# Performance work log

Measured on AMD Instinct MI355X. Metric: run time of the kernel, lower is better.

Reference implementation:

```python
import jax, jax.numpy as jnp
import numpy as np

# dims: B jets, K routed slots per jet, S particles, D embed, E experts, H heads
B, K, S, D, E, H = 512, 2, 128, 128, 4, 8
F = 4 * D  # ffn_dim
MAXN = 1.0 - 1e-5  # Poincare ball (c=1) max norm for projx


def _n(x):
    return jnp.sqrt(jnp.clip(jnp.sum(x * x, axis=-1, keepdims=True), 1e-15))


def expmap0(u):
    n = _n(u)
    return jnp.tanh(n) * u / n


def logmap0(x):
    n = _n(x)
    return jnp.arctanh(jnp.minimum(n, MAXN)) * x / n


def projx(x):
    n = _n(x)
    return jnp.where(n > MAXN, x * (MAXN / n), x)


def mobius_add(x, y):
    xy = jnp.sum(x * y, axis=-1, keepdims=True)
    x2 = jnp.sum(x * x, axis=-1, keepdims=True)
    y2 = jnp.sum(y * y, axis=-1, keepdims=True)
    num = (1.0 + 2.0 * xy + y2) * x + (1.0 - x2) * y
    den = 1.0 + 2.0 * xy + x2 * y2
    return num / jnp.clip(den, 1e-15)


def layernorm(x, g, b):
    m = jnp.mean(x, axis=-1, keepdims=True)
    v = jnp.mean((x - m) ** 2, axis=-1, keepdims=True)
    return g * (x - m) / jnp.sqrt(v + 1e-5) + b


def man_linear(x, W, b):
    # Manifold_Linear: mobius matvec == expmap0(W @ logmap0(x)), then mobius bias, projx
    return projx(mobius_add(expmap0(logmap0(x) @ W.T), expmap0(b)))


def mob_relu(x):
    # Mob_Act(ReLU): expmap0(relu(logmap0(x)))
    return expmap0(jax.nn.relu(logmap0(x)))


def setup_inputs():
    key = jax.random.key(0)
    ks = jax.random.split(key, 16)
    features = expmap0(0.05 * jax.random.normal(ks[0], (B, K, S, D), jnp.float32))
    # K distinct expert ids per sample (original .nonzero().item() assumes uniqueness)
    expert_indices = jnp.argsort(jax.random.uniform(ks[1], (B, E)), axis=1)[:, :K].astype(jnp.int32)
    pm = jax.random.uniform(ks[2], (B, S)) < 0.2
    pm = pm.at[:, 0].set(False)  # keep at least one valid token per row
    w = lambda k, shp, sc: sc * jax.random.normal(k, shp, jnp.float32)
    s = 1.0 / np.sqrt(D)
    sf = 1.0 / np.sqrt(F)
    return dict(
        features=features, expert_indices=expert_indices, padding_mask=pm,
        ln1_g=jnp.ones((E, D)), ln1_b=jnp.zeros((E, D)),
        ln2_g=jnp.ones((E, D)), ln2_b=jnp.zeros((E, D)),
        wq=w(ks[3], (E, D, D), s), bq=w(ks[4], (E, D), 0.02),
        wk=w(ks[5], (E, D, D), s), bk=w(ks[6], (E, D), 0.02),
        wv=w(ks[7], (E, D, D), s), bv=w(ks[8], (E, D), 0.02),
        wo=w(ks[9], (E, D, D), s), bo=w(ks[10], (E, D), 0.02),
        fc1_w=w(ks[11], (E, F, D), s), fc1_b=w(ks[12], (E, F), 0.02),
        fc2_w=w(ks[13], (E, D, F), sf), fc2_b=w(ks[14], (E, D), 0.02),
    )


def _mha(x, Wq, bq, Wk, bk, Wv, bv, Wo, bo, pad_bias):
    b, s, d = x.shape
    hd = d // H
    q = logmap0(man_linear(x, Wq, bq)).reshape(b, s, H, hd)
    k = logmap0(man_linear(x, Wk, bk)).reshape(b, s, H, hd)
    v = logmap0(man_linear(x, Wv, bv)).reshape(b, s, H, hd)
    scores = jnp.einsum('bqhd,bkhd->bhqk', q, k) * (1.0 / np.sqrt(hd)) + pad_bias
    att = jax.nn.softmax(scores, axis=-1)
    ctx = jnp.einsum('bhqk,bkhd->bqhd', att, v).reshape(b, s, d)
    return man_linear(expmap0(ctx), Wo, bo)


def _expert(x, e, P, pad_bias):
    res = x
    h = expmap0(layernorm(logmap0(x), P['ln1_g'][e], P['ln1_b'][e]))
    h = projx(_mha(h, P['wq'][e], P['bq'][e], P['wk'][e], P['bk'][e],
                   P['wv'][e], P['bv'][e], P['wo'][e], P['bo'][e], pad_bias))
    x = projx(mobius_add(h, res))
    res = x
    h = projx(expmap0(layernorm(logmap0(x), P['ln2_g'][e], P['ln2_b'][e])))
    h = projx(mob_relu(man_linear(h, P['fc1_w'][e], P['fc1_b'][e])))
    h = mob_relu(man_linear(h, P['fc2_w'][e], P['fc2_b'][e]))
    return projx(mobius_add(h, res))


def reference(features, expert_indices, padding_mask,
              ln1_g, ln1_b, ln2_g, ln2_b,
              wq, bq, wk, bk, wv, bv, wo, bo,
              fc1_w, fc1_b, fc2_w, fc2_b):
    P = dict(ln1_g=ln1_g, ln1_b=ln1_b, ln2_g=ln2_g, ln2_b=ln2_b,
             wq=wq, bq=bq, wk=wk, bk=bk, wv=wv, bv=bv, wo=wo, bo=bo,
             fc1_w=fc1_w, fc1_b=fc1_b, fc2_w=fc2_w, fc2_b=fc2_b)
    pad_bias = jnp.where(padding_mask, -1e9, 0.0)[:, None, None, :]  # [B,1,1,S]
    outs = []
    for e in range(E):  # small fixed expert loop (distinct params)
        sel = expert_indices == e  # [B,K]
        present = jnp.any(sel, axis=1)  # [B]
        slot = jnp.argmax(sel, axis=1)  # [B]
        x = jnp.take_along_axis(features, slot[:, None, None, None], axis=1)[:, 0]  # [B,S,D]
        y = _expert(x, e, P, pad_bias)
        outs.append(jnp.where(present[:, None, None], y, 0.0))
    return jnp.stack(outs, axis=1)  # [B,E,S,D]; zero rows where expert not routed
```

## Files before the change

kernel.cpp:

```cpp
#include <hip/hip_runtime.h>
#include <stdint.h>

#define SS 128
#define DD 128
#define EE 4
#define HH 8
#define HDIM 16
#define FF 512
#define BB 512
#define KK 2
#define NTASK (BB*KK)
#define MAXNF 0.99999f
#define NW3 786432

typedef unsigned short u16;
typedef unsigned int u32;

typedef __attribute__((ext_vector_type(8))) short s8v;
typedef __attribute__((ext_vector_type(4))) float f4v;

#define MFMA32(a,b,c) __builtin_amdgcn_mfma_f32_16x16x32_bf16(a,b,c,0,0,0)

__device__ __forceinline__ float bf2f(u16 h){ return __uint_as_float(((u32)h)<<16); }
__device__ __forceinline__ u16 f2bf(float f){
  u32 x = __float_as_uint(f);
  u32 r = x + 0x7FFFu + ((x>>16)&1u);
  return (u16)(r>>16);
}
__device__ __forceinline__ float bfl(u32 u){ return __uint_as_float(u<<16); }
__device__ __forceinline__ float bfh(u32 u){ return __uint_as_float(u & 0xFFFF0000u); }

__device__ __forceinline__ float wsum(float v){
  #pragma unroll
  for(int off=32; off>0; off>>=1) v += __shfl_xor(v, off, 64);
  return v;
}
__device__ __forceinline__ float wmax(float v){
  #pragma unroll
  for(int off=32; off>0; off>>=1) v = fmaxf(v, __shfl_xor(v, off, 64));
  return v;
}
__device__ __forceinline__ float rsum16(float v){
  #pragma unroll
  for(int off=8; off>0; off>>=1) v += __shfl_xor(v, off, 64);
  return v;
}
__device__ __forceinline__ float artanhf_(float x){ return 0.5f*logf((1.f+x)/(1.f-x)); }

__device__ __forceinline__ u32 cvtpk(float a, float b){
  u32 r; asm("v_cvt_pk_bf16_f32 %0, %1, %2" : "=v"(r) : "v"(a), "v"(b)); return r;
}
__device__ __forceinline__ void split2(float a, float b, u32& H, u32& M, u32& L){
  H = cvtpk(a,b);
  float ra = a - bfl(H), rb = b - bfh(H);
  M = cvtpk(ra,rb);
  float sa = ra - bfl(M), sb = rb - bfh(M);
  L = cvtpk(sa,sb);
}
__device__ __forceinline__ void split8(const float* v, s8v& H, s8v& M, s8v& L){
  union { u32 w[4]; s8v s; } uh, um, ul;
  #pragma unroll
  for(int p=0;p<4;++p){
    u32 a,bq2,c; split2(v[2*p], v[2*p+1], a, bq2, c);
    uh.w[p]=a; um.w[p]=bq2; ul.w[p]=c;
  }
  H=uh.s; M=um.s; L=ul.s;
}
__device__ __forceinline__ s8v sel8(int c, s8v a, s8v b){ return c ? a : b; }

__device__ __forceinline__ u32 xf32(int row, int colf){
  return (u32)row*512u + (((u32)colf*4u) ^ (((u32)row&7u)<<4));
}
__device__ __forceinline__ u32 xfr_(int row, int colf){
  return (u32)row*2048u + (((u32)colf*4u) ^ (((u32)row&7u)<<4));
}

__device__ __forceinline__ void mkA512(const char* T, int row, int colf, int hm, s8v& A1, s8v& A2){
  float va[8];
  float4 v0 = *(const float4*)(T + xf32(row, colf));
  float4 v1 = *(const float4*)(T + xf32(row, colf+4));
  va[0]=v0.x; va[1]=v0.y; va[2]=v0.z; va[3]=v0.w;
  va[4]=v1.x; va[5]=v1.y; va[6]=v1.z; va[7]=v1.w;
  s8v H,M,L; split8(va, H,M,L);
  A1 = sel8(hm, H, M);
  A2 = sel8(hm, L, H);
}
__device__ __forceinline__ void mkA2048(const char* T, int row, int colf, int hm, s8v& A1, s8v& A2){
  float va[8];
  float4 v0 = *(const float4*)(T + xfr_(row, colf));
  float4 v1 = *(const float4*)(T + xfr_(row, colf+4));
  va[0]=v0.x; va[1]=v0.y; va[2]=v0.z; va[3]=v0.w;
  va[4]=v1.x; va[5]=v1.y; va[6]=v1.z; va[7]=v1.w;
  s8v H,M,L; split8(va, H,M,L);
  A1 = sel8(hm, H, M);
  A2 = sel8(hm, L, H);
}

template<typename T> __device__ __forceinline__ float ldv(const T* p){
  if constexpr (sizeof(T)==2) return bf2f(*(const u16*)p);
  else return *(const float*)p;
}
template<typename T> __device__ __forceinline__ void stv(T* p, float v){
  if constexpr (sizeof(T)==2) *(u16*)p = f2bf(v);
  else *(float*)p = v;
}
template<typename T> __device__ __forceinline__ void loadrow(const T* p, float* w){
  if constexpr (sizeof(T)==2){
    const uint4* q=(const uint4*)p;
    #pragma unroll
    for(int r=0;r<16;++r){
      uint4 t=q[r];
      w[r*8+0]=bfl(t.x); w[r*8+1]=bfh(t.x);
      w[r*8+2]=bfl(t.y); w[r*8+3]=bfh(t.y);
      w[r*8+4]=bfl(t.z); w[r*8+5]=bfh(t.z);
      w[r*8+6]=bfl(t.w); w[r*8+7]=bfh(t.w);
    }
  } else {
    const float4* q=(const float4*)p;
    #pragma unroll
    for(int r=0;r<32;++r){ float4 t=q[r]; w[r*4]=t.x; w[r*4+1]=t.y; w[r*4+2]=t.z; w[r*4+3]=t.w; }
  }
}
__device__ __forceinline__ float dotrow(const float* __restrict__ w, const float* __restrict__ u){
  float a0=0.f,a1=0.f,a2=0.f,a3=0.f;
  #pragma unroll
  for(int i=0;i<128;i+=4){
    a0+=w[i]*u[i]; a1+=w[i+1]*u[i+1]; a2+=w[i+2]*u[i+2]; a3+=w[i+3]*u[i+3];
  }
  return (a0+a1)+(a2+a3);
}

template<int NPL> __device__ __forceinline__ float vnorm(const float* v){
  float s=0.f;
  #pragma unroll
  for(int i=0;i<NPL;++i) s += v[i]*v[i];
  s = wsum(s);
  return sqrtf(fmaxf(s, 1e-15f));
}
template<int NPL> __device__ __forceinline__ void f_logmap0(float* v){
  float n = vnorm<NPL>(v);
  float sc = artanhf_(fminf(n, MAXNF))/n;
  #pragma unroll
  for(int i=0;i<NPL;++i) v[i]*=sc;
}
template<int NPL> __device__ __forceinline__ void f_expmap0(float* v){
  float n = vnorm<NPL>(v);
  float sc = tanhf(n)/n;
  #pragma unroll
  for(int i=0;i<NPL;++i) v[i]*=sc;
}
template<int NPL> __device__ __forceinline__ void f_projx(float* v){
  float n = vnorm<NPL>(v);
  if(n > MAXNF){
    float sc = MAXNF/n;
    #pragma unroll
    for(int i=0;i<NPL;++i) v[i]*=sc;
  }
}
template<int NPL> __device__ __forceinline__ void f_mobius_add(float* x, const float* y){
  float xy=0.f, x2=0.f, y2=0.f;
  #pragma unroll
  for(int i=0;i<NPL;++i){ xy+=x[i]*y[i]; x2+=x[i]*x[i]; y2+=y[i]*y[i]; }
  xy=wsum(xy); x2=wsum(x2); y2=wsum(y2);
  float cx = 1.f + 2.f*xy + y2;
  float cy = 1.f - x2;
  float den = fmaxf(1.f + 2.f*xy + x2*y2, 1e-15f);
  float inv = 1.f/den;
  #pragma unroll
  for(int i=0;i<NPL;++i) x[i] = (cx*x[i] + cy*y[i])*inv;
}
template<int NPL> __device__ __forceinline__ void f_layernorm(float* v, const float* g, const float* b){
  const float invD = 1.f/(float)(NPL*64);
  float m=0.f;
  #pragma unroll
  for(int i=0;i<NPL;++i) m += v[i];
  m = wsum(m)*invD;
  float s2=0.f;
  #pragma unroll
  for(int i=0;i<NPL;++i){ v[i]-=m; s2 += v[i]*v[i]; }
  s2 = wsum(s2)*invD;
  float inv = 1.f/sqrtf(s2+1e-5f);
  #pragma unroll
  for(int i=0;i<NPL;++i) v[i] = g[i]*(v[i]*inv) + b[i];
}

template<int NPL> __device__ __forceinline__ float vnorm16(const float* v){
  float s=0.f;
  #pragma unroll
  for(int i=0;i<NPL;++i) s += v[i]*v[i];
  s = rsum16(s);
  return sqrtf(fmaxf(s, 1e-15f));
}
template<int NPL> __device__ __forceinline__ void f16_logmap0(float* v){
  float n = vnorm16<NPL>(v);
  float sc = artanhf_(fminf(n, MAXNF))/n;
  #pragma unroll
  for(int i=0;i<NPL;++i) v[i]*=sc;
}
template<int NPL> __device__ __forceinline__ void f16_expmap0(float* v){
  float n = vnorm16<NPL>(v);
  float sc = tanhf(n)/n;
  #pragma unroll
  for(int i=0;i<NPL;++i) v[i]*=sc;
}
template<int NPL> __device__ __forceinline__ void f16_projx(float* v){
  float n = vnorm16<NPL>(v);
  if(n > MAXNF){
    float sc = MAXNF/n;
    #pragma unroll
    for(int i=0;i<NPL;++i) v[i]*=sc;
  }
}
template<int NPL> __device__ __forceinline__ void f16_mobius_add(float* x, const float* y){
  float xy=0.f, x2=0.f, y2=0.f;
  #pragma unroll
  for(int i=0;i<NPL;++i){ xy+=x[i]*y[i]; x2+=x[i]*x[i]; y2+=y[i]*y[i]; }
  xy=rsum16(xy); x2=rsum16(x2); y2=rsum16(y2);
  float cx = 1.f + 2.f*xy + y2;
  float cy = 1.f - x2;
  float den = fmaxf(1.f + 2.f*xy + x2*y2, 1e-15f);
  float inv = 1.f/den;
  #pragma unroll
  for(int i=0;i<NPL;++i) x[i] = (cx*x[i] + cy*y[i])*inv;
}
template<int NPL> __device__ __forceinline__ void f16_layernorm(float* v, const float* g, const float* b){
  const float invD = 1.f/(float)(NPL*16);
  float m=0.f;
  #pragma unroll
  for(int i=0;i<NPL;++i) m += v[i];
  m = rsum16(m)*invD;
  float s2=0.f;
  #pragma unroll
  for(int i=0;i<NPL;++i){ v[i]-=m; s2 += v[i]*v[i]; }
  s2 = rsum16(s2)*invD;
  float inv = 1.f/sqrtf(s2+1e-5f);
  #pragma unroll
  for(int i=0;i<NPL;++i) v[i] = g[i]*(v[i]*inv) + b[i];
}

__global__ void prep_kernel(const u16* __restrict__ feat16,
                            const unsigned char* __restrict__ mask,
                            float* __restrict__ mbias, int* __restrict__ flag){
  __shared__ int s_stats, s_max, s_nan;
  if(threadIdx.x==0){ s_stats=0; s_max=0; s_nan=0; }
  __syncthreads();
  int c=0;
  for(int i=threadIdx.x; i<131072; i+=blockDim.x){
    u16 v = feat16[i];
    if(((v>>7)&0xFFu)==0xFFu) c++;
  }
  if(c) atomicAdd(&s_nan, c);
  int lstats=0, lmax=0;
  for(int i=threadIdx.x; i<BB*SS; i+=blockDim.x){
    int v = mask[i];
    if(v){
      lmax = v>lmax ? v : lmax;
      if((i&3)==1) lstats|=1;
      if((i&3)!=0) lstats|=2;
    }
  }
  if(lstats) atomicOr(&s_stats, lstats);
  atomicMax(&s_max, lmax);
  __syncthreads();
  if(threadIdx.x==0) *flag = (s_nan>0) ? 1 : 0;
  int mode;
  if(s_max<=1) mode = (s_stats&2) ? 0 : 1;
  else         mode = (s_stats&1) ? 2 : 3;
  for(int i=threadIdx.x; i<BB*SS; i+=blockDim.x){
    bool m2;
    if(mode==0)      m2 = mask[i]!=0;
    else if(mode==1) m2 = ((const int*)mask)[i]!=0;
    else if(mode==2) m2 = ((const u16*)mask)[i]!=0;
    else             m2 = ((((const u32*)mask)[i])<<1)!=0;
    mbias[i] = m2 ? -1e9f : 0.f;
  }
}

template<typename T>
__global__ void zero_nr(const int* __restrict__ flag, const int* __restrict__ eidx, T* __restrict__ out){
  const int want = (sizeof(T)==4) ? 1 : 0;
  if(*flag != want) return;
  for(int slab=blockIdx.x; slab<BB*EE; slab+=gridDim.x){
    int b = slab>>2, e = slab&3;
    if(eidx[b*KK]==e || eidx[b*KK+1]==e) continue;
    T* p = out + (size_t)slab*(SS*DD);
    for(int i=threadIdx.x; i<SS*DD; i+=blockDim.x){
      if constexpr (sizeof(T)==2) p[i] = (T)0; else p[i] = 0.f;
    }
  }
}

__global__ void wsplit_kernel(const int* __restrict__ flag,
                              const float* __restrict__ wq, const float* __restrict__ wk,
                              const float* __restrict__ wv, const float* __restrict__ wo,
                              const float* __restrict__ f1w, const float* __restrict__ f2w,
                              u16* __restrict__ wsp){
  if(*flag != 1) return;
  int i = blockIdx.x*256 + threadIdx.x;
  if(i >= NW3) return;
  float x;
  if(i < 65536)       x = wq[i];
  else if(i < 131072) x = wk[i-65536];
  else if(i < 196608) x = wv[i-131072];
  else if(i < 262144) x = wo[i-196608];
  else if(i < 524288) x = f1w[i-262144];
  else                x = f2w[i-524288];
  u32 H,M,L; split2(x,x,H,M,L);
  wsp[i]         = (u16)H;
  wsp[NW3 + i]   = (u16)M;
  wsp[2*NW3 + i] = (u16)L;
}

__global__ __launch_bounds__(512)
void moe_f32(const int* __restrict__ flag,
             const float* __restrict__ feat, const int* __restrict__ eidx,
             const float* __restrict__ mbias,
             const float* __restrict__ ln1g, const float* __restrict__ ln1b,
             const float* __restrict__ ln2g, const float* __restrict__ ln2b,
             const float* __restrict__ bq, const float* __restrict__ bk_,
             const float* __restrict__ bv, const float* __restrict__ bo,
             const float* __restrict__ f1b, const float* __restrict__ f2b,
             const u16* __restrict__ wsp,
             float* __restrict__ out, int ntask)
{
  if(*flag != 1) return;

  __shared__ __align__(16) char LB[163840];
  char* UF  = LB;
  char* R2  = LB + 65536;
  char* SX  = LB + 131072;

  const int tid = threadIdx.x;
  const int lane = tid & 63;
  const int w    = tid >> 6;
  const int ll   = lane & 15;
  const int hl   = lane >> 4;
  const int hm   = (hl < 2);

  for(int task = blockIdx.x; task < ntask; task += gridDim.x){
    __syncthreads();
    const int b = task >> 1, slot = task & 1;
    const int e  = eidx[b*KK + slot];
    const int eo = eidx[b*KK + (slot^1)];
    int used = (1<<e)|(1<<eo), sp = 0, cnt = 0;
    #pragma unroll
    for(int t2=0;t2<4;++t2){ if(!((used>>t2)&1)){ if(cnt==slot) sp=t2; cnt++; } }
    const float* X = feat + (size_t)task * (SS*DD);
    float* own   = out + ((size_t)(b*EE+e )) * (SS*DD);
    float* spare = out + ((size_t)(b*EE+sp)) * (SS*DD);

    {
      float g1[2],b1[2];
      float2 t0;
      t0 = *(const float2*)(ln1g + e*DD + 2*lane); g1[0]=t0.x; g1[1]=t0.y;
      t0 = *(const float2*)(ln1b + e*DD + 2*lane); b1[0]=t0.x; b1[1]=t0.y;
      for(int r=0;r<16;++r){
        int t = w*16 + r;
        float2 xv = *(const float2*)(X + t*DD + 2*lane);
        float v[2] = {xv.x, xv.y};
        f_logmap0<2>(v);
        f_layernorm<2>(v, g1, b1);
        f_expmap0<2>(v);
        f_logmap0<2>(v);
        float2 o2; o2.x=v[0]; o2.y=v[1];
        *(float2*)(UF + xf32(t, 2*lane)) = o2;
      }
    }
    __syncthreads();

    {
      float ebq8[8], ebk8[8], ebv8[8];
      #pragma unroll
      for(int n=0;n<8;++n){
        ebq8[n] = bq [e*DD + n*16 + ll];
        ebk8[n] = bk_[e*DD + n*16 + ll];
        ebv8[n] = bv [e*DD + n*16 + ll];
      }
      f16_expmap0<8>(ebq8); f16_expmap0<8>(ebk8); f16_expmap0<8>(ebv8);

      #pragma unroll
      for(int m=0;m<3;++m){
        const u32 tb = (u32)m*65536u + (u32)e*16384u;
        s8v A1v[8], A2v[8];
        #pragma unroll
        for(int c=0;c<8;++c)
          mkA512(UF, w*16+ll, c*16 + (hl&1)*8, hm, A1v[c], A2v[c]);
        f4v acc[8];
        #pragma unroll
        for(int n=0;n<8;++n){ acc[n][0]=0.f; acc[n][1]=0.f; acc[n][2]=0.f; acc[n][3]=0.f; }
        #pragma unroll
        for(int n=0;n<8;++n){
          u32 nrow = (u32)(n*16 + ll);
          #pragma unroll
          for(int c=0;c<8;++c){
            u32 koff = c*16 + (hl&1)*8;
            s8v B1 = *(const s8v*)(wsp + tb + nrow*128 + koff);
            s8v B2 = *(const s8v*)(wsp + (hm?2:1)*NW3 + tb + nrow*128 + koff);
            s8v B3 = sel8(hm, B1, B2);
            acc[n] = MFMA32(A1v[c], B1, acc[n]);
            acc[n] = MFMA32(A1v[c], B2, acc[n]);
            acc[n] = MFMA32(A2v[c], B3, acc[n]);
          }
        }
        #pragma unroll
        for(int i=0;i<4;++i){
          int r = w*16 + hl*4 + i;
          float v[8];
          #pragma unroll
          for(int n=0;n<8;++n) v[n] = acc[n][i];
          f16_expmap0<8>(v);
          float eb[8];
          #pragma unroll
          for(int n=0;n<8;++n) eb[n] = (m==0) ? ebq8[n] : (m==1) ? ebk8[n] : ebv8[n];
          f16_mobius_add<8>(v, eb);
          f16_projx<8>(v);
          f16_logmap0<8>(v);
          if(m==0){
            #pragma unroll
            for(int n=0;n<8;++n) spare[(size_t)r*DD + n*16 + ll] = v[n];
          } else if(m==1){
            #pragma unroll
            for(int n=0;n<8;++n) *(float*)(R2 + xf32(r, n*16 + ll)) = v[n];
          } else {
            #pragma unroll
            for(int n=0;n<8;++n) own[(size_t)r*DD + n*16 + ll] = v[n];
          }
        }
      }
    }
    __syncthreads();

    {
      float mb_reg[8];
      #pragma unroll
      for(int nt=0;nt<8;++nt) mb_reg[nt] = mbias[b*SS + nt*16 + ll];

      for(int h=0; h<HH; ++h){
        {
          int tok = tid & 127, dq = tid >> 7;
          float4 vv = *(const float4*)(R2 + xf32(tok, h*16 + dq*4));
          u32 H0,M0,L0,H1,M1,L1;
          split2(vv.x,vv.y,H0,M0,L0); split2(vv.z,vv.w,H1,M1,L1);
          u32 o = (u32)tok*48u + (u32)dq*8u;
          *(u32*)(SX + 0*6144 + o) = H0; *(u32*)(SX + 0*6144 + o + 4) = H1;
          *(u32*)(SX + 1*6144 + o) = M0; *(u32*)(SX + 1*6144 + o + 4) = M1;
          *(u32*)(SX + 2*6144 + o) = L0; *(u32*)(SX + 2*6144 + o + 4) = L1;
        }
        __syncthreads();
        float qa[8];
        {
          float4 q0 = *(const float4*)(spare + (w*16+ll)*DD + h*16 + (hl&1)*8);
          float4 q1 = *(const float4*)(spare + (w*16+ll)*DD + h*16 + (hl&1)*8 + 4);
          qa[0]=q0.x; qa[1]=q0.y; qa[2]=q0.z; qa[3]=q0.w;
          qa[4]=q1.x; qa[5]=q1.y; qa[6]=q1.z; qa[7]=q1.w;
        }
        s8v QH,QM,QL; split8(qa, QH,QM,QL);
        s8v qA1 = sel8(hm, QH, QM);
        s8v qA2 = sel8(hm, QL, QH);
        f4v sc[8];
        #pragma unroll
        for(int nt=0;nt<8;++nt){
          u32 o = (u32)(nt*16+ll)*48u + (u32)(hl&1)*16u;
          s8v B1 = *(const s8v*)(SX + 0*6144 + o);
          s8v B2 = *(const s8v*)(SX + (hm?2:1)*6144 + o);
          s8v B3 = sel8(hm, B1, B2);
          f4v z = {0.f,0.f,0.f,0.f};
          z = MFMA32(qA1, B1, z);
          z = MFMA32(qA1, B2, z);
          z = MFMA32(qA2, B3, z);
          sc[nt] = z;
        }
        __syncthreads();
        #pragma unroll
        for(int i=0;i<4;++i){
          float p8[8]; float mx = -3e38f;
          #pragma unroll
          for(int nt=0;nt<8;++nt){ p8[nt] = sc[nt][i]*0.25f + mb_reg[nt]; mx = fmaxf(mx, p8[nt]); }
          #pragma unroll
          for(int o=1;o<16;o<<=1) mx = fmaxf(mx, __shfl_xor(mx, o, 64));
          float dn = 0.f;
          #pragma unroll
          for(int nt=0;nt<8;++nt){ p8[nt] = expf(p8[nt]-mx); dn += p8[nt]; }
          #pragma unroll
          for(int o=1;o<16;o<<=1) dn += __shfl_xor(dn, o, 64);
          float inv = 1.f/dn;
          #pragma unroll
          for(int nt=0;nt<8;++nt)
            *(float*)(UF + xf32(w*16 + hl*4 + i, nt*16 + ll)) = p8[nt]*inv;
        }
        f4v ca = {0.f,0.f,0.f,0.f};
        #pragma unroll
        for(int c=0;c<8;++c){
          float pa[8];
          {
            float4 p0 = *(const float4*)(UF + xf32(w*16+ll, c*16 + (hl&1)*8));
            float4 p1 = *(const float4*)(UF + xf32(w*16+ll, c*16 + (hl&1)*8 + 4));
            pa[0]=p0.x; pa[1]=p0.y; pa[2]=p0.z; pa[3]=p0.w;
            pa[4]=p1.x; pa[5]=p1.y; pa[6]=p1.z; pa[7]=p1.w;
          }
          s8v PH,PM,PL; split8(pa, PH,PM,PL);
          s8v pA1 = sel8(hm, PH, PM);
          s8v pA2 = sel8(hm, PL, PH);
          float va[8];
          {
            int kbase = c*16 + (hl&1)*8;
            #pragma unroll
            for(int j=0;j<8;++j)
              va[j] = own[(size_t)(kbase+j)*DD + h*16 + ll];
          }
          s8v VH,VM,VL; split8(va, VH,VM,VL);
          s8v vB2 = sel8(hm, VL, VM);
          s8v vB3 = sel8(hm, VH, VM);
          ca = MFMA32(pA1, VH, ca);
          ca = MFMA32(pA1, vB2, ca);
          ca = MFMA32(pA2, vB3, ca);
        }
        #pragma unroll
        for(int i=0;i<4;++i)
          *(float*)(R2 + xf32(w*16 + hl*4 + i, h*16 + ll)) = ca[i];
      }
    }
    __syncthreads();

    for(int r=0;r<16;++r){
      int t = w*16 + r;
      float2 cc2 = *(const float2*)(R2 + xf32(t, 2*lane));
      float v[2] = {cc2.x, cc2.y};
      f_expmap0<2>(v);
      f_logmap0<2>(v);
      float2 o2; o2.x=v[0]; o2.y=v[1];
      *(float2*)(UF + xf32(t, 2*lane)) = o2;
    }

    {
      float ebo8[8], g28[8], b28[8];
      #pragma unroll
      for(int n=0;n<8;++n){
        ebo8[n] = bo  [e*DD + n*16 + ll];
        g28[n]  = ln2g[e*DD + n*16 + ll];
        b28[n]  = ln2b[e*DD + n*16 + ll];
      }
      f16_expmap0<8>(ebo8);

      const u32 tb = 196608u + (u32)e*16384u;
      s8v A1v[8], A2v[8];
      #pragma unroll
      for(int c=0;c<8;++c)
        mkA512(UF, w*16+ll, c*16 + (hl&1)*8, hm, A1v[c], A2v[c]);
      f4v acc[8];
      #pragma unroll
      for(int n=0;n<8;++n){ acc[n][0]=0.f; acc[n][1]=0.f; acc[n][2]=0.f; acc[n][3]=0.f; }
      #pragma unroll
      for(int n=0;n<8;++n){
        u32 nrow = (u32)(n*16 + ll);
        #pragma unroll
        for(int c=0;c<8;++c){
          u32 koff = c*16 + (hl&1)*8;
          s8v B1 = *(const s8v*)(wsp + tb + nrow*128 + koff);
          s8v B2 = *(const s8v*)(wsp + (hm?2:1)*NW3 + tb + nrow*128 + koff);
          s8v B3 = sel8(hm, B1, B2);
          acc[n] = MFMA32(A1v[c], B1, acc[n]);
          acc[n] = MFMA32(A1v[c], B2, acc[n]);
          acc[n] = MFMA32(A2v[c], B3, acc[n]);
        }
      }
      #pragma unroll
      for(int i=0;i<4;++i){
        int r = w*16 + hl*4 + i;
        float v[8];
        #pragma unroll
        for(int n=0;n<8;++n) v[n] = acc[n][i];
        f16_expmap0<8>(v);
        f16_mobius_add<8>(v, ebo8);
        f16_projx<8>(v);
        f16_projx<8>(v);
        float res[8];
        #pragma unroll
        for(int n=0;n<8;++n) res[n] = X[(size_t)r*DD + n*16 + ll];
        f16_mobius_add<8>(v, res);
        f16_projx<8>(v);
        #pragma unroll
        for(int n=0;n<8;++n) own[(size_t)r*DD + n*16 + ll] = v[n];
        f16_logmap0<8>(v);
        f16_layernorm<8>(v, g28, b28);
        f16_expmap0<8>(v);
        f16_projx<8>(v);
        f16_logmap0<8>(v);
        #pragma unroll
        for(int n=0;n<8;++n) *(float*)(UF + xf32(r, n*16 + ll)) = v[n];
      }
    }
    __syncthreads();

    {
      float ebf1[8], ebf2[2];
      {
        float2 t0;
        #pragma unroll
        for(int j2=0;j2<4;++j2){
          t0 = *(const float2*)(f1b + e*FF + 2*lane + 128*j2); ebf1[2*j2]=t0.x; ebf1[2*j2+1]=t0.y;
        }
        f_expmap0<8>(ebf1);
        t0 = *(const float2*)(f2b + e*DD + 2*lane); ebf2[0]=t0.x; ebf2[1]=t0.y; f_expmap0<2>(ebf2);
      }
      for(int tc=0; tc<4; ++tc){
        const int t0i = tc*32;
        {
          #pragma unroll
          for(int mt=0; mt<2; ++mt){
            int arow = t0i + mt*16 + ll;
            s8v A1v[8], A2v[8];
            #pragma unroll
            for(int c=0;c<8;++c)
              mkA512(UF, arow, c*16 + (hl&1)*8, hm, A1v[c], A2v[c]);
            #pragma unroll
            for(int n4=0;n4<4;++n4){
              u32 nrow = (u32)(w*64 + n4*16 + ll);
              f4v acc = {0.f,0.f,0.f,0.f};
              #pragma unroll
              for(int c=0;c<8;++c){
                u32 koff = c*16 + (hl&1)*8;
                s8v B1 = *(const s8v*)(wsp + 262144u + (u32)e*65536u + nrow*128 + koff);
                s8v B2 = *(const s8v*)(wsp + (hm?2:1)*NW3 + 262144u + (u32)e*65536u + nrow*128 + koff);
                s8v B3 = sel8(hm, B1, B2);
                acc = MFMA32(A1v[c], B1, acc);
                acc = MFMA32(A1v[c], B2, acc);
                acc = MFMA32(A2v[c], B3, acc);
              }
              #pragma unroll
              for(int i=0;i<4;++i)
                *(float*)(R2 + xfr_(mt*16 + hl*4 + i, w*64 + n4*16 + ll)) = acc[i];
            }
          }
        }
        __syncthreads();
        for(int rr=0; rr<4; ++rr){
          int lr = w*4 + rr;
          float v[8];
          #pragma unroll
          for(int j2=0;j2<4;++j2){
            float2 pp = *(const float2*)(R2 + xfr_(lr, 2*lane + 128*j2));
            v[2*j2]=pp.x; v[2*j2+1]=pp.y;
          }
          f_expmap0<8>(v);
          f_mobius_add<8>(v, ebf1);
          f_projx<8>(v);
          f_logmap0<8>(v);
          #pragma unroll
          for(int i=0;i<8;++i) v[i] = fmaxf(v[i], 0.f);
          f_expmap0<8>(v);
          f_projx<8>(v);
          f_logmap0<8>(v);
          #pragma unroll
          for(int j2=0;j2<4;++j2){
            float2 o2; o2.x=v[2*j2]; o2.y=v[2*j2+1];
            *(float2*)(R2 + xfr_(lr, 2*lane + 128*j2)) = o2;
          }
        }
        __syncthreads();
        {
          u32 nrow = (u32)(w*16 + ll);
          #pragma unroll
          for(int mt=0; mt<2; ++mt){
            f4v ga = {0.f,0.f,0.f,0.f};
            #pragma unroll
            for(int grp=0; grp<4; ++grp){
              s8v A1v[8], A2v[8];
              #pragma unroll
              for(int cc=0;cc<8;++cc)
                mkA2048(R2, mt*16 + ll, (grp*8+cc)*16 + (hl&1)*8, hm, A1v[cc], A2v[cc]);
              #pragma unroll
              for(int cc=0;cc<8;++cc){
                int c = grp*8 + cc;
                u32 koff = c*16 + (hl&1)*8;
                s8v B1 = *(const s8v*)(wsp + 524288u + (u32)e*65536u + nrow*512 + koff);
                s8v B2 = *(const s8v*)(wsp + (hm?2:1)*NW3 + 524288u + (u32)e*65536u + nrow*512 + koff);
                s8v B3 = sel8(hm, B1, B2);
                ga = MFMA32(A1v[cc], B1, ga);
                ga = MFMA32(A1v[cc], B2, ga);
                ga = MFMA32(A2v[cc], B3, ga);
              }
            }
            #pragma unroll
            for(int i=0;i<4;++i)
              *(float*)(SX + xf32(mt*16 + hl*4 + i, w*16 + ll)) = ga[i];
          }
        }
        __syncthreads();
        for(int rr=0; rr<4; ++rr){
          int lr = w*4 + rr; int gt = t0i + lr;
          float v[2];
          v[0] = *(const float*)(SX + xf32(lr, 2*lane));
          v[1] = *(const float*)(SX + xf32(lr, 2*lane+1));
          f_expmap0<2>(v);
          f_mobius_add<2>(v, ebf2);
          f_projx<2>(v);
          f_logmap0<2>(v);
          v[0]=fmaxf(v[0],0.f); v[1]=fmaxf(v[1],0.f);
          f_expmap0<2>(v);
          float2 xx = *(const float2*)(own + gt*DD + 2*lane);
          float x1v[2] = {xx.x, xx.y};
          f_mobius_add<2>(v, x1v);
          f_projx<2>(v);
          float2 o2; o2.x=v[0]; o2.y=v[1];
          *(float2*)(own + gt*DD + 2*lane) = o2;
        }
        __syncthreads();
      }
    }

    {
      float4 z4 = {0.f,0.f,0.f,0.f};
      for(int i=tid; i<4096; i+=512) *(float4*)(spare + 4*i) = z4;
    }
  }
}

template<typename T>
__global__ __launch_bounds__(256)
void moe_kernel(const int* __restrict__ flag,
                const T* __restrict__ feat, const int* __restrict__ eidx,
                const float* __restrict__ mbias,
                const T* __restrict__ ln1g, const T* __restrict__ ln1b,
                const T* __restrict__ ln2g, const T* __restrict__ ln2b,
                const T* __restrict__ wq, const T* __restrict__ bq,
                const T* __restrict__ wk, const T* __restrict__ bk_,
                const T* __restrict__ wv, const T* __restrict__ bv,
                const T* __restrict__ wo, const T* __restrict__ bo,
                const T* __restrict__ f1w, const T* __restrict__ f1b,
                const T* __restrict__ f2w, const T* __restrict__ f2b,
                T* __restrict__ out, float* __restrict__ ws, int ntask)
{
  const int want = (sizeof(T)==4) ? 1 : 0;
  if(*flag != want) return;

  __shared__ float U[SS*DD];
  const int tid  = threadIdx.x;
  const int lane = tid & 63;
  const int wid  = tid >> 6;
  float* T0 = ws + (size_t)blockIdx.x * (4*SS*DD);
  float* T1 = T0 + SS*DD;
  float* T2 = T1 + SS*DD;
  float* T3 = T2 + SS*DD;

  for(int task = blockIdx.x; task < ntask; task += gridDim.x){
    __syncthreads();
    const int b = task >> 1;
    const int e = eidx[b*KK + (task & 1)];
    const T* X = feat + (size_t)task * (SS*DD);

    for(int r=0;r<32;++r){
      int t = wid*32 + r;
      float v[2];
      v[0]=ldv(&X[t*DD+lane]); v[1]=ldv(&X[t*DD+lane+64]);
      f_logmap0<2>(v);
      float g[2], bb[2];
      g[0]=ldv(&ln1g[e*DD+lane]);  g[1]=ldv(&ln1g[e*DD+lane+64]);
      bb[0]=ldv(&ln1b[e*DD+lane]); bb[1]=ldv(&ln1b[e*DD+lane+64]);
      f_layernorm<2>(v,g,bb);
      f_expmap0<2>(v);
      f_logmap0<2>(v);
      U[t*DD+lane]=v[0]; U[t*DD+lane+64]=v[1];
    }
    __syncthreads();

    {
      int j = tid & 127, tg = tid >> 7;
      for(int m=0;m<3;++m){
        const T* Wm = (m==0?wq : m==1?wk : wv) + (size_t)e*DD*DD + (size_t)j*DD;
        float* Ym = (m==0?T0 : m==1?T1 : T2);
        float w[128];
        loadrow(Wm, w);
        for(int tt=0;tt<64;++tt){
          int t = tg*64+tt;
          Ym[t*DD+j] = dotrow(w, &U[t*DD]);
        }
      }
    }
    __syncthreads();

    for(int m=0;m<3;++m){
      const T* bias = (m==0?bq : m==1?bk_ : bv) + e*DD;
      float* Y = (m==0?T0 : m==1?T1 : T2);
      for(int r=0;r<32;++r){
        int t = wid*32+r;
        float v[2]; v[0]=Y[t*DD+lane]; v[1]=Y[t*DD+lane+64];
        f_expmap0<2>(v);
        float ebv2[2]; ebv2[0]=ldv(&bias[lane]); ebv2[1]=ldv(&bias[lane+64]);
        f_expmap0<2>(ebv2);
        f_mobius_add<2>(v, ebv2);
        f_projx<2>(v);
        f_logmap0<2>(v);
        Y[t*DD+lane]=v[0]; Y[t*DD+lane+64]=v[1];
      }
    }
    __syncthreads();

    {
      const float* mb = mbias + b*SS;
      for(int h=0; h<HH; ++h){
        for(int r=0;r<32;++r){
          int t = wid*32+r;
          float q16[16];
          #pragma unroll
          for(int i=0;i<16;++i) q16[i] = T0[t*DD + h*HDIM + i];
          int k0 = lane, k1 = lane+64;
          float s0=0.f, s1=0.f;
          #pragma unroll
          for(int i=0;i<16;++i){
            s0 += q16[i]*T1[k0*DD + h*HDIM + i];
            s1 += q16[i]*T1[k1*DD + h*HDIM + i];
          }
          s0 = s0*0.25f + mb[k0];
          s1 = s1*0.25f + mb[k1];
          float mx = wmax(fmaxf(s0,s1));
          float p0 = expf(s0-mx), p1 = expf(s1-mx);
          float dn = wsum(p0+p1);
          p0 /= dn; p1 /= dn;
          float part[16];
          #pragma unroll
          for(int i=0;i<16;++i)
            part[i] = p0*T2[k0*DD+h*HDIM+i] + p1*T2[k1*DD+h*HDIM+i];
          #pragma unroll
          for(int off=1; off<64; off<<=1){
            #pragma unroll
            for(int i=0;i<16;++i) part[i] += __shfl_xor(part[i], off, 64);
          }
          if(lane==0){
            #pragma unroll
            for(int i=0;i<16;++i) T0[t*DD + h*HDIM + i] = part[i];
          }
        }
      }
    }
    __syncthreads();

    for(int r=0;r<32;++r){
      int t=wid*32+r;
      float v[2]; v[0]=T0[t*DD+lane]; v[1]=T0[t*DD+lane+64];
      f_expmap0<2>(v);
      f_logmap0<2>(v);
      U[t*DD+lane]=v[0]; U[t*DD+lane+64]=v[1];
    }
    __syncthreads();

    {
      int j=tid&127, tg=tid>>7;
      float w[128];
      loadrow(wo + (size_t)e*DD*DD + (size_t)j*DD, w);
      for(int tt=0;tt<64;++tt){
        int t=tg*64+tt;
        T1[t*DD+j] = dotrow(w, &U[t*DD]);
      }
    }
    __syncthreads();

    for(int r=0;r<32;++r){
      int t=wid*32+r;
      float v[2]; v[0]=T1[t*DD+lane]; v[1]=T1[t*DD+lane+64];
      f_expmap0<2>(v);
      float ebv2[2]; ebv2[0]=ldv(&bo[e*DD+lane]); ebv2[1]=ldv(&bo[e*DD+lane+64]);
      f_expmap0<2>(ebv2);
      f_mobius_add<2>(v, ebv2);
      f_projx<2>(v);
      f_projx<2>(v);
      float res[2]; res[0]=ldv(&X[t*DD+lane]); res[1]=ldv(&X[t*DD+lane+64]);
      f_mobius_add<2>(v, res);
      f_projx<2>(v);
      T3[t*DD+lane]=v[0]; T3[t*DD+lane+64]=v[1];
      f_logmap0<2>(v);
      float g2[2], b2[2];
      g2[0]=ldv(&ln2g[e*DD+lane]); g2[1]=ldv(&ln2g[e*DD+lane+64]);
      b2[0]=ldv(&ln2b[e*DD+lane]); b2[1]=ldv(&ln2b[e*DD+lane+64]);
      f_layernorm<2>(v,g2,b2);
      f_expmap0<2>(v);
      f_projx<2>(v);
      f_logmap0<2>(v);
      U[t*DD+lane]=v[0]; U[t*DD+lane+64]=v[1];
    }
    __syncthreads();

    float* HID = T0;
    for(int tc=0; tc<2; ++tc){
      for(int pass=0;pass<2;++pass){
        int f = pass*256 + tid;
        float w[128];
        loadrow(f1w + (size_t)e*FF*DD + (size_t)f*DD, w);
        for(int tt=0;tt<64;++tt){
          HID[tt*FF+f] = dotrow(w, &U[(tc*64+tt)*DD]);
        }
      }
      __syncthreads();
      for(int r=0;r<16;++r){
        int t = wid*16+r;
        float v[8];
        #pragma unroll
        for(int i=0;i<8;++i) v[i]=HID[t*FF+lane+64*i];
        f_expmap0<8>(v);
        float ebv8[8];
        #pragma unroll
        for(int i=0;i<8;++i) ebv8[i]=ldv(&f1b[e*FF+lane+64*i]);
        f_expmap0<8>(ebv8);
        f_mobius_add<8>(v, ebv8);
        f_projx<8>(v);
        f_logmap0<8>(v);
        #pragma unroll
        for(int i=0;i<8;++i) v[i]=fmaxf(v[i],0.f);
        f_expmap0<8>(v);
        f_projx<8>(v);
        f_logmap0<8>(v);
        #pragma unroll
        for(int i=0;i<8;++i) HID[t*FF+lane+64*i]=v[i];
      }
      __syncthreads();
      {
        int j=tid&127, tg=tid>>7;
        for(int fc=0;fc<4;++fc){
          float w[128];
          loadrow(f2w + (size_t)e*DD*FF + (size_t)j*FF + fc*128, w);
          for(int tt=0;tt<32;++tt){
            int t=tg*32+tt;
            float acc = dotrow(w, HID + t*FF + fc*128);
            if(fc==0) T2[t*DD+j]=acc; else T2[t*DD+j]+=acc;
          }
        }
      }
      __syncthreads();
      for(int r=0;r<16;++r){
        int t=wid*16+r; int gt = tc*64+t;
        float v[2]; v[0]=T2[t*DD+lane]; v[1]=T2[t*DD+lane+64];
        f_expmap0<2>(v);
        float ebv2[2]; ebv2[0]=ldv(&f2b[e*DD+lane]); ebv2[1]=ldv(&f2b[e*DD+lane+64]);
        f_expmap0<2>(ebv2);
        f_mobius_add<2>(v, ebv2);
        f_projx<2>(v);
        f_logmap0<2>(v);
        v[0]=fmaxf(v[0],0.f); v[1]=fmaxf(v[1],0.f);
        f_expmap0<2>(v);
        float x1v[2]; x1v[0]=T3[gt*DD+lane]; x1v[1]=T3[gt*DD+lane+64];
        f_mobius_add<2>(v, x1v);
        f_projx<2>(v);
        T* op = out + ((size_t)(b*EE+e)*SS + gt)*DD;
        stv(&op[lane],    v[0]);
        stv(&op[lane+64], v[1]);
      }
      __syncthreads();
    }
  }
}

extern "C" void kernel_launch(void* const* d_in, const int* in_sizes, int n_in,
                              void* d_out, int out_size, void* d_ws, size_t ws_size,
                              hipStream_t stream){
  const void* feat = d_in[0];
  const int* eidx = (const int*)d_in[1];
  const unsigned char* pmask = (const unsigned char*)d_in[2];
  float* ws = (float*)d_ws;

  int* flag = (int*)ws;
  float* mbias = ws + 16;
  float* tiles = ws + 16 + BB*SS;
  u16* wsp = (u16*)(ws + 16 + BB*SS);
  const size_t WSP_F32 = (size_t)(3*NW3)/2;

  long wsf = (long)(ws_size/sizeof(float));
  long avail_old = wsf - (16 + BB*SS);
  long remain = wsf - (long)(16 + BB*SS) - (long)WSP_F32;

  int G = (int)(avail_old / (long)(4*SS*DD));
  if(G > NTASK) G = NTASK;
  if(G < 1) G = 1;
  int G2 = 256;
  if(G2 > NTASK) G2 = NTASK;
  bool newpath = (remain >= 0);

  prep_kernel<<<1,256,0,stream>>>((const u16*)feat, pmask, mbias, flag);
  zero_nr<u16>  <<<2048,256,0,stream>>>(flag, eidx, (u16*)d_out);
  zero_nr<float><<<2048,256,0,stream>>>(flag, eidx, (float*)d_out);

  if(newpath){
    wsplit_kernel<<<(NW3+255)/256,256,0,stream>>>(flag,
      (const float*)d_in[7], (const float*)d_in[9], (const float*)d_in[11], (const float*)d_in[13],
      (const float*)d_in[15], (const float*)d_in[17], wsp);
    moe_f32<<<G2,512,0,stream>>>(flag, (const float*)d_in[0], eidx, mbias,
      (const float*)d_in[3], (const float*)d_in[4], (const float*)d_in[5], (const float*)d_in[6],
      (const float*)d_in[8], (const float*)d_in[10], (const float*)d_in[12], (const float*)d_in[14],
      (const float*)d_in[16], (const float*)d_in[18],
      wsp, (float*)d_out, NTASK);
  }

  #define ARGS(T_) flag, (const T_*)d_in[0], eidx, mbias, \
    (const T_*)d_in[3], (const T_*)d_in[4], (const T_*)d_in[5], (const T_*)d_in[6], \
    (const T_*)d_in[7], (const T_*)d_in[8], (const T_*)d_in[9], (const T_*)d_in[10], \
    (const T_*)d_in[11], (const T_*)d_in[12], (const T_*)d_in[13], (const T_*)d_in[14], \
    (const T_*)d_in[15], (const T_*)d_in[16], (const T_*)d_in[17], (const T_*)d_in[18], \
    (T_*)d_out, tiles, NTASK
  moe_kernel<u16><<<G,256,0,stream>>>(ARGS(u16));
  if(!newpath){
    moe_kernel<float><<<G,256,0,stream>>>(ARGS(float));
  }
  #undef ARGS
}
```

Baseline: 3.837 ms.

## Pre-split K into LDS bf16 planes and keep attention context in registers

K is written to LDS once as three bf16 planes (high/mid/low), which removes the per-head re-split of K and the two block-wide barriers per head. The LN1 prologue and the post-attention expmap/logmap now use the same per-wave MFMA row mapping, so each wave only reads rows it wrote itself and one barrier goes away. The per-head context accumulators stay in registers (ctxr) instead of passing through LDS. The cost is higher register pressure from the fully unrolled head loop, which may lower occupancy or spill.

```diff
diff --git a/kernel.cpp b/kernel.cpp
--- a/kernel.cpp
+++ b/kernel.cpp
@@ -73,6 +73,9 @@
 }
 __device__ __forceinline__ u32 xfr_(int row, int colf){
   return (u32)row*2048u + (((u32)colf*4u) ^ (((u32)row&7u)<<4));
+}
+__device__ __forceinline__ u32 xbh(int row, int colb){
+  return (u32)row*256u + (((u32)colb*2u) ^ (((u32)row&7u)<<4));
 }
 
 __device__ __forceinline__ void mkA512(const char* T, int row, int colf, int hm, s8v& A1, s8v& A2){
@@ -327,6 +330,7 @@
 
   __shared__ __align__(16) char LB[163840];
   char* UF  = LB;
+  char* K3  = LB + 65536;
   char* R2  = LB + 65536;
   char* SX  = LB + 131072;
 
@@ -350,23 +354,26 @@
     float* spare = out + ((size_t)(b*EE+sp)) * (SS*DD);
 
     {
-      float g1[2],b1[2];
-      float2 t0;
-      t0 = *(const float2*)(ln1g + e*DD + 2*lane); g1[0]=t0.x; g1[1]=t0.y;
-      t0 = *(const float2*)(ln1b + e*DD + 2*lane); b1[0]=t0.x; b1[1]=t0.y;
-      for(int r=0;r<16;++r){
-        int t = w*16 + r;
-        float2 xv = *(const float2*)(X + t*DD + 2*lane);
-        float v[2] = {xv.x, xv.y};
-        f_logmap0<2>(v);
-        f_layernorm<2>(v, g1, b1);
-        f_expmap0<2>(v);
-        f_logmap0<2>(v);
-        float2 o2; o2.x=v[0]; o2.y=v[1];
-        *(float2*)(UF + xf32(t, 2*lane)) = o2;
-      }
-    }
-    __syncthreads();
+      float g1f[8], b1f[8];
+      #pragma unroll
+      for(int n=0;n<8;++n){
+        g1f[n] = ln1g[e*DD + n*16 + ll];
+        b1f[n] = ln1b[e*DD + n*16 + ll];
+      }
+      #pragma unroll
+      for(int i=0;i<4;++i){
+        int r = w*16 + hl*4 + i;
+        float v[8];
+        #pragma unroll
+        for(int n=0;n<8;++n) v[n] = X[(size_t)r*DD + n*16 + ll];
+        f16_logmap0<8>(v);
+        f16_layernorm<8>(v, g1f, b1f);
+        f16_expmap0<8>(v);
+        f16_logmap0<8>(v);
+        #pragma unroll
+        for(int n=0;n<8;++n) *(float*)(UF + xf32(r, n*16 + ll)) = v[n];
+      }
+    }
 
     {
       float ebq8[8], ebk8[8], ebv8[8];
@@ -420,7 +427,13 @@
             for(int n=0;n<8;++n) spare[(size_t)r*DD + n*16 + ll] = v[n];
           } else if(m==1){
             #pragma unroll
-            for(int n=0;n<8;++n) *(float*)(R2 + xf32(r, n*16 + ll)) = v[n];
+            for(int n=0;n<8;++n){
+              u32 H,M,L; split2(v[n], v[n], H, M, L);
+              u32 o = xbh(r, n*16 + ll);
+              *(u16*)(K3 + 0*32768 + o) = (u16)H;
+              *(u16*)(K3 + 1*32768 + o) = (u16)M;
+              *(u16*)(K3 + 2*32768 + o) = (u16)L;
+            }
           } else {
             #pragma unroll
             for(int n=0;n<8;++n) own[(size_t)r*DD + n*16 + ll] = v[n];
@@ -430,23 +443,14 @@
     }
     __syncthreads();
 
+    f4v ctxr[8];
     {
       float mb_reg[8];
       #pragma unroll
       for(int nt=0;nt<8;++nt) mb_reg[nt] = mbias[b*SS + nt*16 + ll];
 
+      #pragma unroll
       for(int h=0; h<HH; ++h){
-        {
-          int tok = tid & 127, dq = tid >> 7;
-          float4 vv = *(const float4*)(R2 + xf32(tok, h*16 + dq*4));
-          u32 H0,M0,L0,H1,M1,L1;
-          split2(vv.x,vv.y,H0,M0,L0); split2(vv.z,vv.w,H1,M1,L1);
-          u32 o = (u32)tok*48u + (u32)dq*8u;
-          *(u32*)(SX + 0*6144 + o) = H0; *(u32*)(SX + 0*6144 + o + 4) = H1;
-          *(u32*)(SX + 1*6144 + o) = M0; *(u32*)(SX + 1*6144 + o + 4) = M1;
-          *(u32*)(SX + 2*6144 + o) = L0; *(u32*)(SX + 2*6144 + o + 4) = L1;
-        }
-        __syncthreads();
         float qa[8];
         {
           float4 q0 = *(const float4*)(spare + (w*16+ll)*DD + h*16 + (hl&1)*8);
@@ -460,9 +464,9 @@
         f4v sc[8];
         #pragma unroll
         for(int nt=0;nt<8;++nt){
-          u32 o = (u32)(nt*16+ll)*48u + (u32)(hl&1)*16u;
-          s8v B1 = *(const s8v*)(SX + 0*6144 + o);
-          s8v B2 = *(const s8v*)(SX + (hm?2:1)*6144 + o);
+          u32 o = xbh(nt*16+ll, h*16 + (hl&1)*8);
+          s8v B1 = *(const s8v*)(K3 + o);
+          s8v B2 = *(const s8v*)(K3 + (hm?2:1)*32768 + o);
           s8v B3 = sel8(hm, B1, B2);
           f4v z = {0.f,0.f,0.f,0.f};
           z = MFMA32(qA1, B1, z);
@@ -470,7 +474,6 @@
           z = MFMA32(qA2, B3, z);
           sc[nt] = z;
         }
-        __syncthreads();
         #pragma unroll
         for(int i=0;i<4;++i){
           float p8[8]; float mx = -3e38f;
@@ -515,21 +518,21 @@
           ca = MFMA32(pA1, vB2, ca);
           ca = MFMA32(pA2, vB3, ca);
         }
-        #pragma unroll
-        for(int i=0;i<4;++i)
-          *(float*)(R2 + xf32(w*16 + hl*4 + i, h*16 + ll)) = ca[i];
-      }
-    }
-    __syncthreads();
-
-    for(int r=0;r<16;++r){
-      int t = w*16 + r;
-      float2 cc2 = *(const float2*)(R2 + xf32(t, 2*lane));
-      float v[2] = {cc2.x, cc2.y};
-      f_expmap0<2>(v);
-      f_logmap0<2>(v);
-      float2 o2; o2.x=v[0]; o2.y=v[1];
-      *(float2*)(UF + xf32(t, 2*lane)) = o2;
+        ctxr[h] = ca;
+      }
+    }
+    __syncthreads();
+
+    #pragma unroll
+    for(int i=0;i<4;++i){
+      int r = w*16 + hl*4 + i;
+      float v[8];
+      #pragma unroll
+      for(int n=0;n<8;++n) v[n] = ctxr[n][i];
+      f16_expmap0<8>(v);
+      f16_logmap0<8>(v);
+      #pragma unroll
+      for(int n=0;n<8;++n) *(float*)(UF + xf32(r, n*16 + ll)) = v[n];
     }
 
     {
```

New measurement: 4.727 ms. 1.23x slower.
